# Kernel tuning notes

Measured on AMD Instinct MI355X. Metric: run time of the kernel, lower is better.

## Reference

```python
import jax, jax.numpy as jnp
import numpy as np
import math

H = 16
D_MODEL = 1024
B, S = 2, 2048

def setup_inputs() -> dict:
    key = jax.random.key(0)
    ks = jax.random.split(key, 7)
    q = jax.random.normal(ks[0], (B, S, D_MODEL), dtype=jnp.float32)
    k = jax.random.normal(ks[1], (B, S, D_MODEL), dtype=jnp.float32)
    v = jax.random.normal(ks[2], (B, S, D_MODEL), dtype=jnp.float32)
    mask = jnp.ones((1, 1, S, S), dtype=jnp.int32)
    sc = 1.0 / math.sqrt(D_MODEL)
    W_Q = jax.random.normal(ks[3], (D_MODEL, D_MODEL), dtype=jnp.float32) * sc
    W_K = jax.random.normal(ks[4], (D_MODEL, D_MODEL), dtype=jnp.float32) * sc
    W_V = jax.random.normal(ks[5], (D_MODEL, D_MODEL), dtype=jnp.float32) * sc
    W_T = jax.random.normal(ks[6], (D_MODEL, D_MODEL), dtype=jnp.float32) * sc
    return {"q": q, "k": k, "v": v, "mask": mask, "W_Q": W_Q, "W_K": W_K, "W_V": W_V, "W_T": W_T}

def reference(q, k, v, mask, W_Q, W_K, W_V, W_T):
    # W matrices stored as (in, out); nn.Linear applies x @ W.T with W (out,in),
    # equivalent here since we treat these directly as projection matrices.
    def split_heads(x):  # [B,S,D] -> [B,H,S,hd]
        Bq, Sq, Dq = x.shape
        return x.reshape(Bq, Sq, H, Dq // H).transpose(0, 2, 1, 3)

    Q = split_heads(q @ W_Q)
    K = split_heads(k @ W_K)
    V = split_heads(v @ W_V)
    d_k = Q.shape[-1]
    score = jnp.einsum("bhqd,bhkd->bhqk", Q, K) / math.sqrt(d_k)
    score = jnp.where(mask == 0, jnp.float32(-1e9), score)
    attn = jax.nn.softmax(score, axis=-1)
    out = jnp.einsum("bhqk,bhkd->bhqd", attn, V)
    out = out.transpose(0, 2, 1, 3).reshape(q.shape[0], q.shape[1], D_MODEL)
    return out @ W_T
```

## Files before the change

kernel.cpp:

```cpp
#include <hip/hip_runtime.h>
#include <hip/hip_bf16.h>
#include <stdint.h>

#define H  16
#define DM 1024
#define BB 2
#define SS 2048
#define HD 64

#define QSCALE 0.18033688011112042f
#define MASKVAL -57.7078f

typedef __attribute__((ext_vector_type(8))) short bf16x8;
typedef __attribute__((ext_vector_type(4))) float f32x4;

__device__ __forceinline__ short f2bf(float f) {
  __hip_bfloat16 h = __float2bfloat16(f);
  return *reinterpret_cast<short*>(&h);
}

__device__ __forceinline__ void load16_lds(const short* g, short* l) {
  __builtin_amdgcn_global_load_lds(
      (const __attribute__((address_space(1))) void*)g,
      (__attribute__((address_space(3))) void*)l, 16, 0, 0);
}

__global__ void transpose_w_kernel(const float* __restrict__ Wq, const float* __restrict__ Wk,
                                   const float* __restrict__ Wv, const float* __restrict__ Wt,
                                   short* __restrict__ dst, int* __restrict__ flag) {
  if (blockIdx.x == 0 && blockIdx.y == 0 && blockIdx.z == 0 &&
      threadIdx.y == 0 && threadIdx.x < 2) flag[threadIdx.x] = 0;
  __shared__ short tile[32][33];
  int z = blockIdx.z;
  const float* src = (z == 0) ? Wq : (z == 1) ? Wk : (z == 2) ? Wv : Wt;
  short* out = dst + (size_t)z * DM * DM;
  int c0 = blockIdx.x * 32, r0 = blockIdx.y * 32;
  int tx = threadIdx.x, ty = threadIdx.y;
  for (int j = 0; j < 4; j++)
    tile[ty + j * 8][tx] = f2bf(src[(size_t)(r0 + ty + j * 8) * DM + c0 + tx]);
  __syncthreads();
  for (int j = 0; j < 4; j++)
    out[(size_t)(c0 + ty + j * 8) * DM + r0 + tx] = tile[tx][ty + j * 8];
}

__global__ void transpose_v_kernel(const short* __restrict__ Vbuf, short* __restrict__ Vt) {
  __shared__ short tile[32][33];
  int bh = blockIdx.z;
  int s0 = blockIdx.x * 32, d0 = blockIdx.y * 32;
  int tx = threadIdx.x, ty = threadIdx.y;
  for (int j = 0; j < 4; j++)
    tile[ty + j * 8][tx] = Vbuf[((size_t)bh * SS + s0 + ty + j * 8) * HD + d0 + tx];
  __syncthreads();
  for (int j = 0; j < 4; j++)
    Vt[((size_t)bh * HD + d0 + ty + j * 8) * SS + s0 + tx] = tile[tx][ty + j * 8];
}

__global__ void convert_mask_kernel(const float* __restrict__ q, const float* __restrict__ k,
                                    const float* __restrict__ v, short* __restrict__ dst,
                                    const int4* __restrict__ mask4, int* __restrict__ flag) {
  int z = blockIdx.z;
  if (z == 3) {
    int idx = blockIdx.x * blockDim.x + threadIdx.x;
    int4 m = mask4[idx];
    if (m.x == 0 || m.y == 0 || m.z == 0 || m.w == 0) atomicOr(flag, 1);
    return;
  }
  const float* src = (z == 0) ? q : (z == 1) ? k : v;
  short* out = dst + (size_t)z * BB * SS * DM;
  size_t i = ((size_t)blockIdx.x * blockDim.x + threadIdx.x) * 4;
  float4 f = *(const float4*)&src[i];
  short tmp[4] = {f2bf(f.x), f2bf(f.y), f2bf(f.z), f2bf(f.w)};
  *(int2*)&out[i] = *(const int2*)tmp;
}

__global__ void flag_init_kernel(int* flag) { if (threadIdx.x < 2) flag[threadIdx.x] = 0; }

__global__ void mask_scan_kernel(const int4* __restrict__ mask4, int n4, int* __restrict__ flag) {
  int idx = blockIdx.x * blockDim.x + threadIdx.x;
  int stride = gridDim.x * blockDim.x;
  int any = 0;
  for (int i = idx; i < n4; i += stride) {
    int4 m = mask4[i];
    if (m.x == 0 || m.y == 0 || m.z == 0 || m.w == 0) any = 1;
  }
  if (any) atomicOr(flag, 1);
}

__global__ void signal_fill_kernel(float* __restrict__ out, int n) {
  int i = blockIdx.x * blockDim.x + threadIdx.x;
  if (i < n) out[i] = 1.0f;
}

template <int AF32>
__device__ __forceinline__ void gemm_fast_body(const void* __restrict__ Av,
                                               const short* __restrict__ Bt,
                                               void* __restrict__ Cv, int mode, float scale) {
  __shared__ __align__(16) short As[128 * 32];
  __shared__ __align__(16) short Bs[128 * 32];
  int m0 = blockIdx.x * 128, n0 = blockIdx.y * 128;
  int t = threadIdx.x;
  int lane = t & 63, w = t >> 6;
  int l16 = lane & 15, quad = lane >> 4;
  int wm = (w >> 1) * 64, wn = (w & 1) * 64;
  f32x4 acc[4][4] = {};

  for (int k0 = 0; k0 < DM; k0 += 32) {
    if (AF32) {
      const float* A = (const float*)Av;
      for (int i = 0; i < 4; i++) {
        int c = t + i * 256;
        int row = c >> 3, seg = c & 7;
        float4 f = *(const float4*)&A[(size_t)(m0 + row) * DM + k0 + seg * 4];
        short tmp[4] = {f2bf(f.x), f2bf(f.y), f2bf(f.z), f2bf(f.w)};
        *(int2*)&As[row * 32 + seg * 4] = *(const int2*)tmp;
      }
    } else {
      const short* A = (const short*)Av;
      for (int i = 0; i < 2; i++) {
        int c = t + i * 256;
        load16_lds(&A[(size_t)(m0 + (c >> 2)) * DM + k0 + (c & 3) * 8], &As[c * 8]);
      }
    }
    for (int i = 0; i < 2; i++) {
      int c = t + i * 256;
      load16_lds(&Bt[(size_t)(n0 + (c >> 2)) * DM + k0 + (c & 3) * 8], &Bs[c * 8]);
    }
    __syncthreads();
    bf16x8 af[4], bfr[4];
    for (int i = 0; i < 4; i++) af[i]  = *(const bf16x8*)&As[(wm + i * 16 + l16) * 32 + quad * 8];
    for (int i = 0; i < 4; i++) bfr[i] = *(const bf16x8*)&Bs[(wn + i * 16 + l16) * 32 + quad * 8];
    for (int mi = 0; mi < 4; mi++)
      for (int ni = 0; ni < 4; ni++)
        acc[mi][ni] = __builtin_amdgcn_mfma_f32_16x16x32_bf16(af[mi], bfr[ni], acc[mi][ni], 0, 0, 0);
    __syncthreads();
  }

  for (int mi = 0; mi < 4; mi++)
    for (int ni = 0; ni < 4; ni++)
      for (int r = 0; r < 4; r++) {
        int m = m0 + wm + mi * 16 + quad * 4 + r;
        int n = n0 + wn + ni * 16 + l16;
        if (mode == 0) {
          short* C = (short*)Cv;
          int b = m >> 11, s = m & (SS - 1);
          int h = n >> 6, d = n & (HD - 1);
          C[(((size_t)(b * H + h) * SS) + s) * HD + d] = f2bf(acc[mi][ni][r] * scale);
        } else {
          float* C = (float*)Cv;
          C[(size_t)m * DM + n] = acc[mi][ni][r];
        }
      }
}

template <int AF32>
__global__ __launch_bounds__(256, 2) void gemm_qkv_fast_kernel(
    const void* __restrict__ A0, const void* __restrict__ A1, const void* __restrict__ A2,
    const short* __restrict__ WTall,
    short* __restrict__ Qb, short* __restrict__ Kb, short* __restrict__ Vb) {
  int z = blockIdx.z;
  const void* A = (z == 0) ? A0 : (z == 1) ? A1 : A2;
  const short* B = WTall + (size_t)z * DM * DM;
  short* C = (z == 0) ? Qb : (z == 1) ? Kb : Vb;
  gemm_fast_body<AF32>(A, B, (void*)C, 0, (z == 0) ? QSCALE : 1.0f);
}

__global__ __launch_bounds__(256, 2) void gemm_out_fast_kernel(
    const short* __restrict__ Obuf, const short* __restrict__ WtT, float* __restrict__ out) {
  gemm_fast_body<0>((const void*)Obuf, WtT, (void*)out, 2, 1.0f);
}

#define LDT 40
#define LDB 136

template <int AF32>
__device__ __forceinline__ void gemm_legacy_body(const void* __restrict__ Av,
                                                 const float* __restrict__ Bm,
                                                 void* __restrict__ Cv, int mode, float scale) {
  __shared__ __align__(16) short As[128 * LDT];
  __shared__ __align__(16) short Bsh[32 * LDB];
  int m0 = blockIdx.x * 128, n0 = blockIdx.y * 128;
  int t = threadIdx.x;
  int lane = t & 63, w = t >> 6;
  int l16 = lane & 15, quad = lane >> 4;
  int wm = (w >> 1) * 64, wn = (w & 1) * 64;
  f32x4 acc[4][4] = {};

  for (int k0 = 0; k0 < DM; k0 += 32) {
    if (AF32) {
      const float* A = (const float*)Av;
      for (int i = 0; i < 4; i++) {
        int c = t + i * 256;
        int row = c >> 3, seg = c & 7;
        float4 f = *(const float4*)&A[(size_t)(m0 + row) * DM + k0 + seg * 4];
        short tmp[4] = {f2bf(f.x), f2bf(f.y), f2bf(f.z), f2bf(f.w)};
        *(int2*)&As[row * LDT + seg * 4] = *(const int2*)tmp;
      }
    } else {
      const short* A = (const short*)Av;
      for (int i = 0; i < 2; i++) {
        int c = t + i * 256;
        int row = c >> 2, seg = c & 3;
        *(int4*)&As[row * LDT + seg * 8] = *(const int4*)&A[(size_t)(m0 + row) * DM + k0 + seg * 8];
      }
    }
    for (int i = 0; i < 4; i++) {
      int c = t + i * 256;
      int krow = c >> 5, nseg = c & 31;
      float4 f = *(const float4*)&Bm[(size_t)(k0 + krow) * DM + n0 + nseg * 4];
      short tmp[4] = {f2bf(f.x), f2bf(f.y), f2bf(f.z), f2bf(f.w)};
      *(int2*)&Bsh[krow * LDB + nseg * 4] = *(const int2*)tmp;
    }
    __syncthreads();
    bf16x8 af[4], bfr[4];
    for (int i = 0; i < 4; i++) af[i] = *(const bf16x8*)&As[(wm + i * 16 + l16) * LDT + quad * 8];
    for (int i = 0; i < 4; i++) {
      bf16x8 tmp;
      for (int j = 0; j < 8; j++) tmp[j] = Bsh[(quad * 8 + j) * LDB + wn + i * 16 + l16];
      bfr[i] = tmp;
    }
    for (int mi = 0; mi < 4; mi++)
      for (int ni = 0; ni < 4; ni++)
        acc[mi][ni] = __builtin_amdgcn_mfma_f32_16x16x32_bf16(af[mi], bfr[ni], acc[mi][ni], 0, 0, 0);
    __syncthreads();
  }

  for (int mi = 0; mi < 4; mi++)
    for (int ni = 0; ni < 4; ni++)
      for (int r = 0; r < 4; r++) {
        int m = m0 + wm + mi * 16 + quad * 4 + r;
        int n = n0 + wn + ni * 16 + l16;
        if (mode == 0) {
          short* C = (short*)Cv;
          int b = m >> 11, s = m & (SS - 1);
          int h = n >> 6, d = n & (HD - 1);
          C[(((size_t)(b * H + h) * SS) + s) * HD + d] = f2bf(acc[mi][ni][r] * scale);
        } else {
          float* C = (float*)Cv;
          C[(size_t)m * DM + n] = acc[mi][ni][r];
        }
      }
}

__global__ __launch_bounds__(256, 2) void gemm_qkv_legacy_kernel(
    const float* __restrict__ q, const float* __restrict__ k, const float* __restrict__ v,
    const float* __restrict__ B0, const float* __restrict__ B1, const float* __restrict__ B2,
    short* __restrict__ Qb, short* __restrict__ Kb, short* __restrict__ Vb) {
  int z = blockIdx.z;
  const float* A = (z == 0) ? q : (z == 1) ? k : v;
  const float* B = (z == 0) ? B0 : (z == 1) ? B1 : B2;
  short* C = (z == 0) ? Qb : (z == 1) ? Kb : Vb;
  gemm_legacy_body<1>((const void*)A, B, (void*)C, 0, (z == 0) ? QSCALE : 1.0f);
}

__global__ __launch_bounds__(256, 2) void gemm_out_legacy_kernel(
    const short* __restrict__ Obuf, const float* __restrict__ Wt, float* __restrict__ out) {
  gemm_legacy_body<0>((const void*)Obuf, Wt, (void*)out, 2, 1.0f);
}

#define LDP 72

__global__ __launch_bounds__(256, 2) void attn128_kernel(
    const short* __restrict__ Q, const short* __restrict__ K,
    const short* __restrict__ Vt, const int* __restrict__ mask,
    const int* __restrict__ flag, short* __restrict__ O) {
  __shared__ __align__(16) short Ks[64 * 64];
  __shared__ __align__(16) short Vs[64 * 64];
  __shared__ __align__(16) short Ps[4][32 * LDP];

  int bh = blockIdx.y;
  int q0 = blockIdx.x * 128;
  int t = threadIdx.x, lane = t & 63, w = t >> 6;
  int l16 = lane & 15, quad = lane >> 4;
  int use_mask = flag[0];

  bf16x8 aq[2][2];
  for (int g = 0; g < 2; g++) {
    const short* qrow = Q + ((size_t)bh * SS + q0 + w * 32 + g * 16 + l16) * HD;
    aq[g][0] = *(const bf16x8*)&qrow[quad * 8];
    aq[g][1] = *(const bf16x8*)&qrow[32 + quad * 8];
  }

  float lsum[2] = {0.f, 0.f};
  f32x4 oacc[2][4] = {};

  const short* Kbase = K  + (size_t)bh * SS * HD;
  const short* Vbase = Vt + (size_t)bh * HD * SS;

  for (int kt = 0; kt < SS / 64; kt++) {
    int kb = kt * 64;
    for (int i = 0; i < 2; i++) {
      int p = t + i * 256;
      int rp = p >> 3, cp = p & 7;
      int lc = cp ^ (rp & 7);
      load16_lds(&Kbase[(size_t)(kb + rp) * HD + lc * 8], &Ks[p * 8]);
      load16_lds(&Vbase[(size_t)rp * SS + kb + lc * 8], &Vs[p * 8]);
    }
    __syncthreads();

    for (int kb2 = 0; kb2 < 4; kb2++) {
      int krow = kb2 * 16 + l16;
      bf16x8 k0 = *(const bf16x8*)&Ks[krow * 64 + ((quad ^ (l16 & 7)) * 8)];
      bf16x8 k1 = *(const bf16x8*)&Ks[krow * 64 + (((quad + 4) ^ (l16 & 7)) * 8)];
      for (int g = 0; g < 2; g++) {
        f32x4 sc = {};
        sc = __builtin_amdgcn_mfma_f32_16x16x32_bf16(k0, aq[g][0], sc, 0, 0, 0);
        sc = __builtin_amdgcn_mfma_f32_16x16x32_bf16(k1, aq[g][1], sc, 0, 0, 0);
        if (use_mask) {
          int qg = q0 + w * 32 + g * 16 + l16;
          for (int r = 0; r < 4; r++) {
            int kg = kb + kb2 * 16 + quad * 4 + r;
            if (mask[(size_t)qg * SS + kg] == 0) sc[r] = MASKVAL;
          }
        }
        float pv[4];
        for (int r = 0; r < 4; r++) {
          pv[r] = __builtin_exp2f(fminf(sc[r], 115.0f));
          lsum[g] += pv[r];
        }
        unsigned u0 = ((unsigned)(unsigned short)f2bf(pv[1]) << 16) | (unsigned short)f2bf(pv[0]);
        unsigned u1 = ((unsigned)(unsigned short)f2bf(pv[3]) << 16) | (unsigned short)f2bf(pv[2]);
        uint2 packed = {u0, u1};
        *(uint2*)&Ps[w][(g * 16 + l16) * LDP + kb2 * 16 + quad * 4] = packed;
      }
    }

    for (int c = 0; c < 2; c++) {
      bf16x8 ap[2];
      for (int g = 0; g < 2; g++)
        ap[g] = *(const bf16x8*)&Ps[w][(g * 16 + l16) * LDP + c * 32 + quad * 8];
      for (int nb2 = 0; nb2 < 4; nb2++) {
        bf16x8 bv = *(const bf16x8*)&Vs[(nb2 * 16 + l16) * 64 + (((c * 4 + quad) ^ (l16 & 7)) * 8)];
        for (int g = 0; g < 2; g++)
          oacc[g][nb2] = __builtin_amdgcn_mfma_f32_16x16x32_bf16(ap[g], bv, oacc[g][nb2], 0, 0, 0);
      }
    }
    __syncthreads();
  }

  for (int g = 0; g < 2; g++) {
    lsum[g] += __shfl_xor(lsum[g], 16);
    lsum[g] += __shfl_xor(lsum[g], 32);
  }

  int b = bh >> 4, h = bh & 15;
  for (int g = 0; g < 2; g++)
    for (int r = 0; r < 4; r++) {
      float inv = 1.0f / __shfl(lsum[g], quad * 4 + r);
      int qg = q0 + w * 32 + g * 16 + quad * 4 + r;
      for (int nb2 = 0; nb2 < 4; nb2++) {
        int d = nb2 * 16 + l16;
        O[((size_t)(b * SS + qg)) * DM + h * HD + d] = f2bf(oacc[g][nb2][r] * inv);
      }
    }
}

__global__ __launch_bounds__(256, 4) void attn64_kernel(
    const short* __restrict__ Q, const short* __restrict__ K,
    const short* __restrict__ V, const int* __restrict__ mask,
    const int* __restrict__ flag, short* __restrict__ O) {
  __shared__ __align__(16) short Ks[64 * 64];
  __shared__ __align__(16) short Vs[64 * 64];
  __shared__ __align__(16) short Ps[4][16 * LDP];

  int bh = blockIdx.y;
  int q0 = blockIdx.x * 64;
  int t = threadIdx.x, lane = t & 63, w = t >> 6;
  int l16 = lane & 15, quad = lane >> 4;
  int use_mask = flag[0];

  const short* qrow = Q + ((size_t)bh * SS + q0 + w * 16 + l16) * HD;
  bf16x8 aq0 = *(const bf16x8*)&qrow[quad * 8];
  bf16x8 aq1 = *(const bf16x8*)&qrow[32 + quad * 8];

  float lsum[4] = {0.f, 0.f, 0.f, 0.f};
  f32x4 oacc[4] = {};

  const short* Kbase = K + (size_t)bh * SS * HD;
  const short* Vbase = V + (size_t)bh * SS * HD;
  int dd = t & 63, h2 = t >> 6;

  for (int kt = 0; kt < SS / 64; kt++) {
    int kb = kt * 64;
    for (int i = 0; i < 2; i++) {
      int p = t + i * 256;
      int rp = p >> 3, cp = p & 7;
      int lc = cp ^ (rp & 7);
      load16_lds(&Kbase[(size_t)(kb + rp) * HD + lc * 8], &Ks[p * 8]);
    }
    for (int sgi = 0; sgi < 2; sgi++) {
      int sg = h2 * 2 + sgi;
      short tmp[8];
      for (int jj = 0; jj < 8; jj++)
        tmp[jj] = Vbase[(size_t)(kb + sg * 8 + jj) * HD + dd];
      *(int4*)&Vs[dd * 64 + ((sg ^ (dd & 7)) * 8)] = *(const int4*)tmp;
    }
    __syncthreads();

    for (int nb = 0; nb < 4; nb++) {
      f32x4 sc = {};
      bf16x8 bk0 = *(const bf16x8*)&Ks[(nb * 16 + l16) * 64 + ((quad ^ (l16 & 7)) * 8)];
      bf16x8 bk1 = *(const bf16x8*)&Ks[(nb * 16 + l16) * 64 + (((quad + 4) ^ (l16 & 7)) * 8)];
      sc = __builtin_amdgcn_mfma_f32_16x16x32_bf16(aq0, bk0, sc, 0, 0, 0);
      sc = __builtin_amdgcn_mfma_f32_16x16x32_bf16(aq1, bk1, sc, 0, 0, 0);
      if (use_mask) {
        int kg = kb + nb * 16 + l16;
        for (int r = 0; r < 4; r++) {
          int qg = q0 + w * 16 + quad * 4 + r;
          if (mask[(size_t)qg * SS + kg] == 0) sc[r] = MASKVAL;
        }
      }
      for (int r = 0; r < 4; r++) {
        float pv = __builtin_exp2f(fminf(sc[r], 115.0f));
        lsum[r] += pv;
        Ps[w][(quad * 4 + r) * LDP + nb * 16 + l16] = f2bf(pv);
      }
    }

    for (int c = 0; c < 2; c++) {
      bf16x8 ap = *(const bf16x8*)&Ps[w][l16 * LDP + c * 32 + quad * 8];
      for (int nb2 = 0; nb2 < 4; nb2++) {
        bf16x8 bv = *(const bf16x8*)&Vs[(nb2 * 16 + l16) * 64 + (((c * 4 + quad) ^ (l16 & 7)) * 8)];
        oacc[nb2] = __builtin_amdgcn_mfma_f32_16x16x32_bf16(ap, bv, oacc[nb2], 0, 0, 0);
      }
    }
    __syncthreads();
  }

  for (int st = 1; st < 16; st <<= 1)
    for (int r = 0; r < 4; r++) lsum[r] += __shfl_xor(lsum[r], st);

  int b = bh >> 4, h = bh & 15;
  for (int r = 0; r < 4; r++) {
    float inv = 1.0f / lsum[r];
    int qg = q0 + w * 16 + quad * 4 + r;
    for (int nb2 = 0; nb2 < 4; nb2++) {
      int d = nb2 * 16 + l16;
      O[((size_t)(b * SS + qg)) * DM + h * HD + d] = f2bf(oacc[nb2][r] * inv);
    }
  }
}

extern "C" void kernel_launch(void* const* d_in, const int* in_sizes, int n_in,
                              void* d_out, int out_size, void* d_ws, size_t ws_size,
                              hipStream_t stream) {
  const float* q    = (const float*)d_in[0];
  const float* k    = (const float*)d_in[1];
  const float* v    = (const float*)d_in[2];
  const int*   mask = (const int*)d_in[3];
  const float* Wq   = (const float*)d_in[4];
  const float* Wk   = (const float*)d_in[5];
  const float* Wv   = (const float*)d_in[6];
  const float* Wt   = (const float*)d_in[7];
  float* out = (float*)d_out;

  char* ws = (char*)d_ws;
  const size_t MB = 1024ull * 1024ull;
  const size_t NEED_A = 66 * MB;
  const size_t NEED_B = 40 * MB + 4096;
  const size_t NEED_C = 32 * MB + 4096;

  if (ws_size >= NEED_A) {
    short* WTall = (short*)(ws);
    short* Qbuf  = (short*)(ws + 8 * MB);
    short* Kbuf  = (short*)(ws + 16 * MB);
    short* Vbuf  = (short*)(ws + 24 * MB);
    short* Obuf  = (short*)(ws + 32 * MB);
    int*   flag  = (int*)(ws + 40 * MB);
    short* Abf   = (short*)(ws + 41 * MB);
    short* Vt    = Abf;

    transpose_w_kernel<<<dim3(32, 32, 4), dim3(32, 8), 0, stream>>>(Wq, Wk, Wv, Wt, WTall, flag);
    convert_mask_kernel<<<dim3(4096, 1, 4), 256, 0, stream>>>(q, k, v, Abf, (const int4*)mask, flag);
    gemm_qkv_fast_kernel<0><<<dim3(BB * SS / 128, DM / 128, 3), 256, 0, stream>>>(
        Abf, Abf + (size_t)BB * SS * DM, Abf + 2ull * BB * SS * DM, WTall, Qbuf, Kbuf, Vbuf);
    transpose_v_kernel<<<dim3(SS / 32, HD / 32, BB * H), dim3(32, 8), 0, stream>>>(Vbuf, Vt);
    attn128_kernel<<<dim3(SS / 128, BB * H), 256, 0, stream>>>(Qbuf, Kbuf, Vt, mask, flag, Obuf);
    gemm_out_fast_kernel<<<dim3(BB * SS / 128, DM / 128), 256, 0, stream>>>(
        Obuf, WTall + 3ull * DM * DM, out);
  } else if (ws_size >= NEED_B) {
    short* WTall = (short*)(ws);
    short* Qbuf  = (short*)(ws + 8 * MB);
    short* Kbuf  = (short*)(ws + 16 * MB);
    short* Vbuf  = (short*)(ws + 24 * MB);
    short* Obuf  = (short*)(ws + 32 * MB);
    int*   flag  = (int*)(ws + 40 * MB);

    transpose_w_kernel<<<dim3(32, 32, 4), dim3(32, 8), 0, stream>>>(Wq, Wk, Wv, Wt, WTall, flag);
    mask_scan_kernel<<<512, 256, 0, stream>>>((const int4*)mask, SS * SS / 4, flag);
    gemm_qkv_fast_kernel<1><<<dim3(BB * SS / 128, DM / 128, 3), 256, 0, stream>>>(
        q, k, v, WTall, Qbuf, Kbuf, Vbuf);
    attn64_kernel<<<dim3(SS / 64, BB * H), 256, 0, stream>>>(Qbuf, Kbuf, Vbuf, mask, flag, Obuf);
    gemm_out_fast_kernel<<<dim3(BB * SS / 128, DM / 128), 256, 0, stream>>>(
        Obuf, WTall + 3ull * DM * DM, out);
  } else if (ws_size >= NEED_C) {
    short* Qbuf = (short*)(ws);
    short* Kbuf = (short*)(ws + 8 * MB);
    short* Vbuf = (short*)(ws + 16 * MB);
    short* Obuf = (short*)(ws + 24 * MB);
    int*   flag = (int*)(ws + 32 * MB);

    flag_init_kernel<<<1, 64, 0, stream>>>(flag);
    mask_scan_kernel<<<512, 256, 0, stream>>>((const int4*)mask, SS * SS / 4, flag);
    gemm_qkv_legacy_kernel<<<dim3(BB * SS / 128, DM / 128, 3), 256, 0, stream>>>(
        q, k, v, Wq, Wk, Wv, Qbuf, Kbuf, Vbuf);
    attn64_kernel<<<dim3(SS / 64, BB * H), 256, 0, stream>>>(Qbuf, Kbuf, Vbuf, mask, flag, Obuf);
    gemm_out_legacy_kernel<<<dim3(BB * SS / 128, DM / 128), 256, 0, stream>>>(Obuf, Wt, out);
  } else {
    signal_fill_kernel<<<(BB * SS * DM + 255) / 256, 256, 0, stream>>>(out, BB * SS * DM);
  }
}
```

Measured before the change: 265.5 us.

## Double-buffer K/V tiles in attention kernel to overlap loads with compute

The attention kernel now keeps two LDS buffers for K and V tiles. The next tile is prefetched with global_load_lds while the current tile is consumed, and the barrier before compute is removed except for the first tile. This is meant to hide global-memory latency behind the MFMA work. It doubles K/V LDS use, which may lower occupancy. The loop still has only one barrier, at the end of each iteration, and that barrier may not wait for the outstanding async LDS loads (vmcnt), so tile reads could race with in-flight loads.

```diff
diff --git a/kernel.cpp b/kernel.cpp
--- a/kernel.cpp
+++ b/kernel.cpp
@@ -263,8 +263,8 @@
     const short* __restrict__ Q, const short* __restrict__ K,
     const short* __restrict__ Vt, const int* __restrict__ mask,
     const int* __restrict__ flag, short* __restrict__ O) {
-  __shared__ __align__(16) short Ks[64 * 64];
-  __shared__ __align__(16) short Vs[64 * 64];
+  __shared__ __align__(16) short Ks[2][64 * 64];
+  __shared__ __align__(16) short Vs[2][64 * 64];
   __shared__ __align__(16) short Ps[4][32 * LDP];
 
   int bh = blockIdx.y;
@@ -286,21 +286,34 @@
   const short* Kbase = K  + (size_t)bh * SS * HD;
   const short* Vbase = Vt + (size_t)bh * HD * SS;
 
+  int p0 = t, p1 = t + 256;
+  int rp0 = p0 >> 3, lc0 = (p0 & 7) ^ (rp0 & 7);
+  int rp1 = p1 >> 3, lc1 = (p1 & 7) ^ (rp1 & 7);
+
+  load16_lds(&Kbase[(size_t)rp0 * HD + lc0 * 8], &Ks[0][p0 * 8]);
+  load16_lds(&Vbase[(size_t)rp0 * SS + lc0 * 8], &Vs[0][p0 * 8]);
+  load16_lds(&Kbase[(size_t)rp1 * HD + lc1 * 8], &Ks[0][p1 * 8]);
+  load16_lds(&Vbase[(size_t)rp1 * SS + lc1 * 8], &Vs[0][p1 * 8]);
+  __syncthreads();
+
   for (int kt = 0; kt < SS / 64; kt++) {
+    int cur = kt & 1;
+    if (kt + 1 < SS / 64) {
+      int kb2g = (kt + 1) * 64;
+      int nxt = cur ^ 1;
+      load16_lds(&Kbase[(size_t)(kb2g + rp0) * HD + lc0 * 8], &Ks[nxt][p0 * 8]);
+      load16_lds(&Vbase[(size_t)rp0 * SS + kb2g + lc0 * 8], &Vs[nxt][p0 * 8]);
+      load16_lds(&Kbase[(size_t)(kb2g + rp1) * HD + lc1 * 8], &Ks[nxt][p1 * 8]);
+      load16_lds(&Vbase[(size_t)rp1 * SS + kb2g + lc1 * 8], &Vs[nxt][p1 * 8]);
+    }
     int kb = kt * 64;
-    for (int i = 0; i < 2; i++) {
-      int p = t + i * 256;
-      int rp = p >> 3, cp = p & 7;
-      int lc = cp ^ (rp & 7);
-      load16_lds(&Kbase[(size_t)(kb + rp) * HD + lc * 8], &Ks[p * 8]);
-      load16_lds(&Vbase[(size_t)rp * SS + kb + lc * 8], &Vs[p * 8]);
-    }
-    __syncthreads();
+    const short* Kc = Ks[cur];
+    const short* Vc = Vs[cur];
 
     for (int kb2 = 0; kb2 < 4; kb2++) {
       int krow = kb2 * 16 + l16;
-      bf16x8 k0 = *(const bf16x8*)&Ks[krow * 64 + ((quad ^ (l16 & 7)) * 8)];
-      bf16x8 k1 = *(const bf16x8*)&Ks[krow * 64 + (((quad + 4) ^ (l16 & 7)) * 8)];
+      bf16x8 k0 = *(const bf16x8*)&Kc[krow * 64 + ((quad ^ (l16 & 7)) * 8)];
+      bf16x8 k1 = *(const bf16x8*)&Kc[krow * 64 + (((quad + 4) ^ (l16 & 7)) * 8)];
       for (int g = 0; g < 2; g++) {
         f32x4 sc = {};
         sc = __builtin_amdgcn_mfma_f32_16x16x32_bf16(k0, aq[g][0], sc, 0, 0, 0);
@@ -329,7 +342,7 @@
       for (int g = 0; g < 2; g++)
         ap[g] = *(const bf16x8*)&Ps[w][(g * 16 + l16) * LDP + c * 32 + quad * 8];
       for (int nb2 = 0; nb2 < 4; nb2++) {
-        bf16x8 bv = *(const bf16x8*)&Vs[(nb2 * 16 + l16) * 64 + (((c * 4 + quad) ^ (l16 & 7)) * 8)];
+        bf16x8 bv = *(const bf16x8*)&Vc[(nb2 * 16 + l16) * 64 + (((c * 4 + quad) ^ (l16 & 7)) * 8)];
         for (int g = 0; g < 2; g++)
           oacc[g][nb2] = __builtin_amdgcn_mfma_f32_16x16x32_bf16(ap[g], bv, oacc[g][nb2], 0, 0, 0);
       }
```

New measurement: 262.9 us. Within noise of the previous version (-0.9%).
